# Performance work log

Hardware: AMD Instinct MI355X
Metric: run time of the kernel (lower is better)

## Reference

```python
import jax, jax.numpy as jnp
import numpy as np
import math

B, T, D = 2, 4096, 1024
H = 16
HEAD_DIM = D // H
CHUNK = 64

def setup_inputs() -> dict:
    key = jax.random.key(0)
    ks = jax.random.split(key, 9)
    s = 1.0 / math.sqrt(D)
    return {
        'x':  jax.random.normal(ks[0], (B, T, D), dtype=jnp.float32),
        'Wq': jax.random.normal(ks[1], (D, D), dtype=jnp.float32) * s,
        'bq': jax.random.normal(ks[2], (D,), dtype=jnp.float32) * 0.01,
        'Wk': jax.random.normal(ks[3], (D, D), dtype=jnp.float32) * s,
        'bk': jax.random.normal(ks[4], (D,), dtype=jnp.float32) * 0.01,
        'Wv': jax.random.normal(ks[5], (D, D), dtype=jnp.float32) * s,
        'bv': jax.random.normal(ks[6], (D,), dtype=jnp.float32) * 0.01,
        'Wo': jax.random.normal(ks[7], (D, D), dtype=jnp.float32) * s,
        'bo': jax.random.normal(ks[8], (D,), dtype=jnp.float32) * 0.01,
    }

def chunked_attention(q, k, v, chunk_size, scale):
    # q,k,v: (B,H,T,hd); causal Q-chunked attention, chunk_size divides T
    Bq, Hq, Tq, hd = q.shape
    S = k.shape[2]
    nc = Tq // chunk_size
    # (nc, B, H, chunk, hd)
    q_chunks = q.reshape(Bq, Hq, nc, chunk_size, hd).transpose(2, 0, 1, 3, 4)
    starts = jnp.arange(nc, dtype=jnp.int32) * chunk_size
    k_pos = jnp.arange(S)

    def body(carry, xs):
        qc, start = xs  # qc: (B,H,chunk,hd)
        scores = jnp.einsum('bhqd,bhkd->bhqk', qc, k) * scale  # (B,H,chunk,S)
        q_pos = start + jnp.arange(chunk_size)
        causal_mask = k_pos[None, :] > q_pos[:, None]  # (chunk,S)
        scores = jnp.where(causal_mask[None, None], -jnp.inf, scores)
        m = jnp.max(scores, axis=-1, keepdims=True)
        m = jnp.where(jnp.isinf(m), jnp.zeros_like(m), m)
        p = jax.nn.softmax(scores - m, axis=-1)
        oc = jnp.einsum('bhqk,bhkd->bhqd', p, v)
        return carry, oc

    _, outs = jax.lax.scan(body, None, (q_chunks, starts))  # (nc,B,H,chunk,hd)
    return outs.transpose(1, 2, 0, 3, 4).reshape(Bq, Hq, Tq, hd)

def reference(x, Wq, bq, Wk, bk, Wv, bv, Wo, bo):
    Bx, Tx, Dx = x.shape
    scale = 1.0 / math.sqrt(HEAD_DIM)

    def proj(W, b):
        y = x @ W.T + b  # torch Linear convention
        return y.reshape(Bx, Tx, H, HEAD_DIM).transpose(0, 2, 1, 3)

    q = proj(Wq, bq)
    k = proj(Wk, bk)
    v = proj(Wv, bv)
    out = chunked_attention(q, k, v, CHUNK, scale)  # (B,H,T,hd)
    out = out.transpose(0, 2, 1, 3).reshape(Bx, Tx, Dx)
    return out @ Wo.T + bo
```

## Files before the change

### kernel.cpp

```cpp
#include <hip/hip_runtime.h>
#include <math.h>

#define B_  2
#define T_  4096
#define D_  1024
#define H_  16
#define HD_ 64
#define M_  8192

using f32x4  = __attribute__((ext_vector_type(4)))  float;
using f32x16 = __attribute__((ext_vector_type(16))) float;
using bfrag  = __attribute__((ext_vector_type(8)))  short;

__device__ __forceinline__ unsigned short f2bf(float f) {
  union { float f; unsigned u; } v; v.f = f;
  unsigned r = v.u + 0x7FFFu + ((v.u >> 16) & 1u);
  return (unsigned short)(r >> 16);
}

__device__ __forceinline__ unsigned cvt_pk(float lo, float hi) {
  unsigned r;
  asm("v_cvt_pk_bf16_f32 %0, %1, %2" : "=v"(r) : "v"(lo), "v"(hi));
  return r;
}

__device__ __forceinline__ void plswap(unsigned &a, unsigned &b) {
  asm("v_permlane32_swap_b32 %0, %1" : "+v"(a), "+v"(b));
}

__device__ __forceinline__ void async16(const void* g, void* l) {
  __builtin_amdgcn_global_load_lds(
      (const __attribute__((address_space(1))) unsigned int*)g,
      (__attribute__((address_space(3))) unsigned int*)l, 16, 0, 0);
}

__global__ __launch_bounds__(256) void convert_all(
    const float* __restrict__ x, const float* __restrict__ wq,
    const float* __restrict__ wk, const float* __restrict__ wv,
    const float* __restrict__ wo, unsigned short* __restrict__ dst)
{
  const size_t NX = (size_t)M_ * D_ / 4;
  const size_t NW = (size_t)D_ * D_ / 4;
  const size_t total = NX + 4 * NW;
  size_t i = (size_t)blockIdx.x * blockDim.x + threadIdx.x;
  size_t stride = (size_t)gridDim.x * blockDim.x;
  for (size_t v = i; v < total; v += stride) {
    const float4* src;
    if (v < NX) {
      src = (const float4*)x + v;
    } else {
      size_t j = v - NX;
      const float* wp = (j < NW) ? wq : (j < 2*NW) ? wk : (j < 3*NW) ? wv : wo;
      src = (const float4*)wp + (j & (NW - 1));
    }
    float4 f = *src;
    ushort4 u;
    u.x = f2bf(f.x); u.y = f2bf(f.y); u.z = f2bf(f.z); u.w = f2bf(f.w);
    *(ushort4*)(dst + v * 4) = u;
  }
}

__global__ __launch_bounds__(256) void gemm_qkv(
    const unsigned short* __restrict__ A,
    const unsigned short* __restrict__ Ww,
    const float* __restrict__ bq, const float* __restrict__ bk,
    const float* __restrict__ bv,
    unsigned short* __restrict__ Qb, unsigned short* __restrict__ Kb,
    unsigned short* __restrict__ Vtb, float qscale)
{
  __shared__ unsigned short a_t[128 * 64];
  __shared__ unsigned short b_t[128 * 64];
  const int tid = threadIdx.x;
  const int lane = tid & 63;
  const int w = tid >> 6;
  const int lo = lane & 15, hi = lane >> 4;
  const int mbase = blockIdx.x * 128;
  const int nbase = blockIdx.y * 128;
  const int wm = w >> 1, wn = w & 1;
  const int K = D_;

  f32x4 acc[4][4];
  #pragma unroll
  for (int m = 0; m < 4; m++)
    #pragma unroll
    for (int n = 0; n < 4; n++) acc[m][n] = f32x4{0.f, 0.f, 0.f, 0.f};

  for (int k0 = 0; k0 < K; k0 += 64) {
    #pragma unroll
    for (int i = 0; i < 4; i++) {
      const int cb = i * 256 + w * 64;
      const int chunk = cb + lane;
      const int row = chunk >> 3, c8 = chunk & 7;
      async16(A  + (size_t)(mbase + row) * K + k0 + c8 * 8, &a_t[cb * 8]);
      async16(Ww + (size_t)(nbase + row) * K + k0 + c8 * 8, &b_t[cb * 8]);
    }
    __syncthreads();
    #pragma unroll
    for (int kk = 0; kk < 2; kk++) {
      bfrag af[4], bf[4];
      #pragma unroll
      for (int m = 0; m < 4; m++)
        af[m] = *(const bfrag*)&a_t[(wm * 64 + m * 16 + lo) * 64 + kk * 32 + hi * 8];
      #pragma unroll
      for (int n = 0; n < 4; n++)
        bf[n] = *(const bfrag*)&b_t[(wn * 64 + n * 16 + lo) * 64 + kk * 32 + hi * 8];
      #pragma unroll
      for (int m = 0; m < 4; m++)
        #pragma unroll
        for (int n = 0; n < 4; n++)
          acc[m][n] = __builtin_amdgcn_mfma_f32_16x16x32_bf16(af[m], bf[n], acc[m][n], 0, 0, 0);
    }
    __syncthreads();
  }

  const int which = nbase >> 10;
  const float* bias = (which == 0) ? bq : (which == 1) ? bk : bv;
  const float osc = (which == 0) ? qscale : 1.0f;
  const int nloc = nbase & 1023;

  float bvv[4];
  #pragma unroll
  for (int n = 0; n < 4; n++) bvv[n] = bias[nloc + wn * 64 + n * 16 + lo];

  #pragma unroll
  for (int m = 0; m < 4; m++) {
    const int rowl = wm * 64 + m * 16 + hi * 4;
    #pragma unroll
    for (int n = 0; n < 4; n++) {
      const int gn = nloc + wn * 64 + n * 16 + lo;
      const int h = gn >> 6, d = gn & 63;
      #pragma unroll
      for (int i = 0; i < 4; i++) {
        const float v = (acc[m][n][i] + bvv[n]) * osc;
        const int gm = mbase + rowl + i;
        const int b = gm >> 12, t = gm & 4095;
        const int bh = b * H_ + h;
        if (which == 0) {
          Qb[(((size_t)bh * T_) + t) * HD_ + d] = f2bf(v);
        } else if (which == 1) {
          const int j = t >> 6, kh = (t >> 5) & 1, l31r = t & 31;
          const int s = d >> 4, h5 = (d >> 3) & 1, e = d & 7;
          Kb[(((size_t)(bh * 64 + j) * 8 + kh * 4 + s) * 512)
             + l31r * 16 + h5 * 8 + e] = f2bf(v);
        } else {
          const int j = t >> 6, kh = (t >> 5) & 1, S = (t >> 4) & 1;
          const int h5 = (t >> 3) & 1, e = t & 7;
          const int dset = d >> 5, l31r = d & 31;
          Vtb[(((size_t)(bh * 64 + j) * 8 + kh * 4 + S * 2 + dset) * 512)
              + l31r * 16 + h5 * 8 + e] = f2bf(v);
        }
      }
    }
  }
}

__global__ __launch_bounds__(256) void gemm_out(
    const unsigned short* __restrict__ A,
    const unsigned short* __restrict__ Bw,
    const float* __restrict__ bias,
    float* __restrict__ out,
    int M, int N, int K)
{
  __shared__ unsigned short a_t[128 * 64];
  __shared__ unsigned short b_t[128 * 64];
  const int tid = threadIdx.x;
  const int lane = tid & 63;
  const int w = tid >> 6;
  const int lo = lane & 15, hi = lane >> 4;
  const int mbase = blockIdx.x * 128;
  const int nbase = blockIdx.y * 128;
  const int wm = w >> 1, wn = w & 1;

  f32x4 acc[4][4];
  #pragma unroll
  for (int m = 0; m < 4; m++)
    #pragma unroll
    for (int n = 0; n < 4; n++) acc[m][n] = f32x4{0.f, 0.f, 0.f, 0.f};

  for (int k0 = 0; k0 < K; k0 += 64) {
    #pragma unroll
    for (int i = 0; i < 4; i++) {
      const int cb = i * 256 + w * 64;
      const int chunk = cb + lane;
      const int row = chunk >> 3, c8 = chunk & 7;
      async16(A  + (size_t)(mbase + row) * K + k0 + c8 * 8, &a_t[cb * 8]);
      async16(Bw + (size_t)(nbase + row) * K + k0 + c8 * 8, &b_t[cb * 8]);
    }
    __syncthreads();
    #pragma unroll
    for (int kk = 0; kk < 2; kk++) {
      bfrag af[4], bf[4];
      #pragma unroll
      for (int m = 0; m < 4; m++)
        af[m] = *(const bfrag*)&a_t[(wm * 64 + m * 16 + lo) * 64 + kk * 32 + hi * 8];
      #pragma unroll
      for (int n = 0; n < 4; n++)
        bf[n] = *(const bfrag*)&b_t[(wn * 64 + n * 16 + lo) * 64 + kk * 32 + hi * 8];
      #pragma unroll
      for (int m = 0; m < 4; m++)
        #pragma unroll
        for (int n = 0; n < 4; n++)
          acc[m][n] = __builtin_amdgcn_mfma_f32_16x16x32_bf16(af[m], bf[n], acc[m][n], 0, 0, 0);
    }
    __syncthreads();
  }

  float bvv[4];
  #pragma unroll
  for (int n = 0; n < 4; n++) bvv[n] = bias[nbase + wn * 64 + n * 16 + lo];

  #pragma unroll
  for (int m = 0; m < 4; m++) {
    const int rowl = wm * 64 + m * 16 + hi * 4;
    #pragma unroll
    for (int n = 0; n < 4; n++) {
      const int gn = nbase + wn * 64 + n * 16 + lo;
      #pragma unroll
      for (int i = 0; i < 4; i++)
        out[(size_t)(mbase + rowl + i) * N + gn] = acc[m][n][i] + bvv[n];
    }
  }
}

__global__ __launch_bounds__(256, 3) void attn_kernel(
    const unsigned short* __restrict__ Qg,
    const unsigned short* __restrict__ Kf,
    const unsigned short* __restrict__ Vf,
    unsigned short* __restrict__ Og)
{
  __shared__ float smrg[2176];
  const int tid = threadIdx.x, lane = tid & 63, w = tid >> 6;
  const int l31 = lane & 31, hi5 = lane >> 5;
  const int bh = blockIdx.x & 31;
  const int qgroup = 63 - (blockIdx.x >> 5);
  const int qhalf = w >> 1, khalf = w & 1;
  const int a = qgroup * 2 + qhalf;
  const int qg_lane = qgroup * 64 + qhalf * 32 + l31;
  const int jw = (a >= khalf) ? ((a - khalf) >> 1) : -1;
  const int b = bh >> 4, h = bh & 15;

  bfrag qf0, qf1, qf2, qf3;
  {
    const unsigned short* qp = Qg + ((size_t)bh * T_ + qg_lane) * HD_ + hi5 * 8;
    qf0 = *(const bfrag*)(qp);
    qf1 = *(const bfrag*)(qp + 16);
    qf2 = *(const bfrag*)(qp + 32);
    qf3 = *(const bfrag*)(qp + 48);
  }

  const int loff = l31 * 16 + hi5 * 8;
  const unsigned short* kp =
      Kf + ((size_t)(bh * 64) * 8 + khalf * 4) * 512 + loff;
  const unsigned short* vp =
      Vf + ((size_t)(bh * 64) * 8 + khalf * 4) * 512 + loff;

  f32x16 o0, o1;
  #pragma unroll
  for (int r = 0; r < 16; r++) { o0[r] = 0.f; o1[r] = 0.f; }
  float l = 0.f;

  bfrag kA0, kA1, kA2, kA3, kB0, kB1, kB2, kB3;
  bfrag vf00, vf01, vf10, vf11;

  #define LOADK(P) do {                                                      \
    P##0 = *(const bfrag*)(kp);                                              \
    P##1 = *(const bfrag*)(kp + 512);                                        \
    P##2 = *(const bfrag*)(kp + 1024);                                       \
    P##3 = *(const bfrag*)(kp + 1536);                                       \
    kp += 4096;                                                              \
  } while (0)

  #define LOADV() do {                                                       \
    vf00 = *(const bfrag*)(vp);                                              \
    vf01 = *(const bfrag*)(vp + 512);                                        \
    vf10 = *(const bfrag*)(vp + 1024);                                       \
    vf11 = *(const bfrag*)(vp + 1536);                                       \
    vp += 4096;                                                              \
  } while (0)

  #define COMPUTE(P, J) do {                                                 \
    f32x16 st;                                                               \
    _Pragma("unroll")                                                        \
    for (int r = 0; r < 16; r++) st[r] = 0.f;                                \
    __builtin_amdgcn_s_setprio(1);                                           \
    st = __builtin_amdgcn_mfma_f32_32x32x16_bf16(P##0, qf0, st, 0, 0, 0);    \
    st = __builtin_amdgcn_mfma_f32_32x32x16_bf16(P##1, qf1, st, 0, 0, 0);    \
    st = __builtin_amdgcn_mfma_f32_32x32x16_bf16(P##2, qf2, st, 0, 0, 0);    \
    st = __builtin_amdgcn_mfma_f32_32x32x16_bf16(P##3, qf3, st, 0, 0, 0);    \
    __builtin_amdgcn_s_setprio(0);                                           \
    if ((J) == jw) {                                                         \
      const int thr = qg_lane - 64 * (J) - 32 * khalf - 4 * hi5;             \
      _Pragma("unroll")                                                      \
      for (int r = 0; r < 16; r++) {                                         \
        const int kl = (r & 3) + 8 * (r >> 2);                               \
        st[r] = (kl > thr) ? -INFINITY : st[r];                              \
      }                                                                      \
    }                                                                        \
    _Pragma("unroll")                                                        \
    for (int r = 0; r < 16; r++) st[r] = exp2f(st[r]);                       \
    {                                                                        \
      float s8[8];                                                           \
      _Pragma("unroll")                                                      \
      for (int r = 0; r < 8; r++) s8[r] = st[r] + st[r + 8];                 \
      float rs = ((s8[0] + s8[4]) + (s8[1] + s8[5])) +                       \
                 ((s8[2] + s8[6]) + (s8[3] + s8[7]));                        \
      rs += __shfl_xor(rs, 32);                                              \
      l += rs;                                                               \
    }                                                                        \
    {                                                                        \
      unsigned pk0 = cvt_pk(st[0], st[1]);                                   \
      unsigned pk1 = cvt_pk(st[2], st[3]);                                   \
      unsigned pk2 = cvt_pk(st[4], st[5]);                                   \
      unsigned pk3 = cvt_pk(st[6], st[7]);                                   \
      plswap(pk0, pk2);                                                      \
      plswap(pk1, pk3);                                                      \
      union { unsigned u[4]; bfrag f; } pb;                                  \
      pb.u[0] = pk0; pb.u[1] = pk1; pb.u[2] = pk2; pb.u[3] = pk3;            \
      __builtin_amdgcn_s_setprio(1);                                         \
      o0 = __builtin_amdgcn_mfma_f32_32x32x16_bf16(vf00, pb.f, o0, 0, 0, 0); \
      o1 = __builtin_amdgcn_mfma_f32_32x32x16_bf16(vf01, pb.f, o1, 0, 0, 0); \
      __builtin_amdgcn_s_setprio(0);                                         \
      pk0 = cvt_pk(st[8], st[9]);                                            \
      pk1 = cvt_pk(st[10], st[11]);                                          \
      pk2 = cvt_pk(st[12], st[13]);                                          \
      pk3 = cvt_pk(st[14], st[15]);                                          \
      plswap(pk0, pk2);                                                      \
      plswap(pk1, pk3);                                                      \
      pb.u[0] = pk0; pb.u[1] = pk1; pb.u[2] = pk2; pb.u[3] = pk3;            \
      __builtin_amdgcn_s_setprio(1);                                         \
      o0 = __builtin_amdgcn_mfma_f32_32x32x16_bf16(vf10, pb.f, o0, 0, 0, 0); \
      o1 = __builtin_amdgcn_mfma_f32_32x32x16_bf16(vf11, pb.f, o1, 0, 0, 0); \
      __builtin_amdgcn_s_setprio(0);                                         \
    }                                                                        \
  } while (0)

  if (jw >= 0) {
    LOADK(kA);
    int j = 0;
    while (true) {
      LOADV();
      if (j < jw) LOADK(kB);
      COMPUTE(kA, j);
      ++j; if (j > jw) break;
      LOADV();
      if (j < jw) LOADK(kA);
      COMPUTE(kB, j);
      ++j; if (j > jw) break;
    }
  }
  #undef LOADK
  #undef LOADV
  #undef COMPUTE

  const int moff = (qhalf * 64 + lane) * 17;
  if (khalf) {
    #pragma unroll
    for (int r = 0; r < 16; r++) smrg[moff + r] = o0[r];
    smrg[moff + 16] = l;
  }
  __syncthreads();
  if (!khalf) {
    #pragma unroll
    for (int r = 0; r < 16; r++) o0[r] += smrg[moff + r];
    l += smrg[moff + 16];
  }
  __syncthreads();
  if (khalf) {
    #pragma unroll
    for (int r = 0; r < 16; r++) smrg[moff + r] = o1[r];
  }
  __syncthreads();
  if (!khalf) {
    #pragma unroll
    for (int r = 0; r < 16; r++) o1[r] += smrg[moff + r];
    const float inv = 1.0f / l;
    unsigned short* orow = Og + ((size_t)(b * T_ + qg_lane)) * D_ + h * HD_;
    #pragma unroll
    for (int r = 0; r < 16; r += 2) {
      const int d0 = (r & 3) + 8 * (r >> 2) + 4 * hi5;
      unsigned u0 = cvt_pk(o0[r] * inv, o0[r + 1] * inv);
      unsigned u1 = cvt_pk(o1[r] * inv, o1[r + 1] * inv);
      *(unsigned*)(orow + d0)      = u0;
      *(unsigned*)(orow + 32 + d0) = u1;
    }
  }
}

extern "C" void kernel_launch(void* const* d_in, const int* in_sizes, int n_in,
                              void* d_out, int out_size, void* d_ws, size_t ws_size,
                              hipStream_t stream)
{
  const float* x  = (const float*)d_in[0];
  const float* Wq = (const float*)d_in[1];
  const float* bq = (const float*)d_in[2];
  const float* Wk = (const float*)d_in[3];
  const float* bk = (const float*)d_in[4];
  const float* Wv = (const float*)d_in[5];
  const float* bv = (const float*)d_in[6];
  const float* Wo = (const float*)d_in[7];
  const float* bo = (const float*)d_in[8];

  unsigned short* ws  = (unsigned short*)d_ws;
  unsigned short* xb  = ws;
  unsigned short* wqb = xb  + (size_t)M_ * D_;
  unsigned short* wkb = wqb + (size_t)D_ * D_;
  unsigned short* wvb = wkb + (size_t)D_ * D_;
  unsigned short* wob = wvb + (size_t)D_ * D_;
  unsigned short* Qb  = wob + (size_t)D_ * D_;
  unsigned short* Kb  = Qb  + (size_t)M_ * D_;
  unsigned short* Vtb = Kb  + (size_t)M_ * D_;
  unsigned short* AOb = Vtb + (size_t)M_ * D_;

  convert_all<<<2048, 256, 0, stream>>>(x, Wq, Wk, Wv, Wo, xb);

  const float qscale = 0.125f * 1.44269504f;
  dim3 gq(M_ / 128, 3072 / 128);
  gemm_qkv<<<gq, 256, 0, stream>>>(xb, wqb, bq, bk, bv, Qb, Kb, Vtb, qscale);

  attn_kernel<<<2048, 256, 0, stream>>>(Qb, Kb, Vtb, AOb);

  dim3 go(M_ / 128, D_ / 128);
  gemm_out<<<go, 256, 0, stream>>>(AOb, wob, bo, (float*)d_out, M_, D_, D_);
}
```

Before: 242.1 us.

## Software-pipeline QK MFMA ahead of softmax/PV in attention loop

Restructures the attention inner loop so the QK^T MFMAs for the next key block are issued before the softmax and PV MFMAs of the current block. This lets matrix work overlap with the exp/convert VALU work. The causal mask is applied only to the final block, outside the steady-state loop, and the row-sum cross-half shuffle is deferred to one shuffle after the loop. Launch bounds are raised to 4 blocks per CU and the double-buffered K registers are dropped to save VGPRs. The risk is register spilling or extra loads of K past the last needed block.

```diff
diff --git a/kernel.cpp b/kernel.cpp
--- a/kernel.cpp
+++ b/kernel.cpp
@@ -28,11 +28,13 @@
   asm("v_permlane32_swap_b32 %0, %1" : "+v"(a), "+v"(b));
 }
 
+
 __device__ __forceinline__ void async16(const void* g, void* l) {
   __builtin_amdgcn_global_load_lds(
       (const __attribute__((address_space(1))) unsigned int*)g,
       (__attribute__((address_space(3))) unsigned int*)l, 16, 0, 0);
 }
+
 
 __global__ __launch_bounds__(256) void convert_all(
     const float* __restrict__ x, const float* __restrict__ wq,
@@ -222,7 +224,7 @@
   }
 }
 
-__global__ __launch_bounds__(256, 3) void attn_kernel(
+__global__ __launch_bounds__(256, 4) void attn_kernel(
     const unsigned short* __restrict__ Qg,
     const unsigned short* __restrict__ Kf,
     const unsigned short* __restrict__ Vf,
@@ -259,14 +261,14 @@
   for (int r = 0; r < 16; r++) { o0[r] = 0.f; o1[r] = 0.f; }
   float l = 0.f;
 
-  bfrag kA0, kA1, kA2, kA3, kB0, kB1, kB2, kB3;
+  bfrag kA0, kA1, kA2, kA3;
   bfrag vf00, vf01, vf10, vf11;
 
-  #define LOADK(P) do {                                                      \
-    P##0 = *(const bfrag*)(kp);                                              \
-    P##1 = *(const bfrag*)(kp + 512);                                        \
-    P##2 = *(const bfrag*)(kp + 1024);                                       \
-    P##3 = *(const bfrag*)(kp + 1536);                                       \
+  #define LOADK() do {                                                       \
+    kA0 = *(const bfrag*)(kp);                                               \
+    kA1 = *(const bfrag*)(kp + 512);                                         \
+    kA2 = *(const bfrag*)(kp + 1024);                                        \
+    kA3 = *(const bfrag*)(kp + 1536);                                        \
     kp += 4096;                                                              \
   } while (0)
 
@@ -278,40 +280,40 @@
     vp += 4096;                                                              \
   } while (0)
 
-  #define COMPUTE(P, J) do {                                                 \
-    f32x16 st;                                                               \
+  #define QKSTEP(ST) do {                                                    \
+    __builtin_amdgcn_s_setprio(1);                                           \
+    ST = __builtin_amdgcn_mfma_f32_32x32x16_bf16(kA0, qf0,                   \
+                                                 (f32x16)(0.0f), 0, 0, 0);   \
+    ST = __builtin_amdgcn_mfma_f32_32x32x16_bf16(kA1, qf1, ST, 0, 0, 0);     \
+    ST = __builtin_amdgcn_mfma_f32_32x32x16_bf16(kA2, qf2, ST, 0, 0, 0);     \
+    ST = __builtin_amdgcn_mfma_f32_32x32x16_bf16(kA3, qf3, ST, 0, 0, 0);     \
+    __builtin_amdgcn_s_setprio(0);                                           \
+  } while (0)
+
+  #define MASK(ST) do {                                                     \
+    const int thr = qg_lane - 64 * jw - 32 * khalf - 4 * hi5;                \
     _Pragma("unroll")                                                        \
-    for (int r = 0; r < 16; r++) st[r] = 0.f;                                \
-    __builtin_amdgcn_s_setprio(1);                                           \
-    st = __builtin_amdgcn_mfma_f32_32x32x16_bf16(P##0, qf0, st, 0, 0, 0);    \
-    st = __builtin_amdgcn_mfma_f32_32x32x16_bf16(P##1, qf1, st, 0, 0, 0);    \
-    st = __builtin_amdgcn_mfma_f32_32x32x16_bf16(P##2, qf2, st, 0, 0, 0);    \
-    st = __builtin_amdgcn_mfma_f32_32x32x16_bf16(P##3, qf3, st, 0, 0, 0);    \
-    __builtin_amdgcn_s_setprio(0);                                           \
-    if ((J) == jw) {                                                         \
-      const int thr = qg_lane - 64 * (J) - 32 * khalf - 4 * hi5;             \
-      _Pragma("unroll")                                                      \
-      for (int r = 0; r < 16; r++) {                                         \
-        const int kl = (r & 3) + 8 * (r >> 2);                               \
-        st[r] = (kl > thr) ? -INFINITY : st[r];                              \
-      }                                                                      \
+    for (int r = 0; r < 16; r++) {                                           \
+      const int kl = (r & 3) + 8 * (r >> 2);                                 \
+      ST[r] = (kl > thr) ? -INFINITY : ST[r];                                \
     }                                                                        \
+  } while (0)
+
+  #define SOFTPV(ST) do {                                                    \
     _Pragma("unroll")                                                        \
-    for (int r = 0; r < 16; r++) st[r] = exp2f(st[r]);                       \
+    for (int r = 0; r < 16; r++) ST[r] = exp2f(ST[r]);                       \
     {                                                                        \
       float s8[8];                                                           \
       _Pragma("unroll")                                                      \
-      for (int r = 0; r < 8; r++) s8[r] = st[r] + st[r + 8];                 \
-      float rs = ((s8[0] + s8[4]) + (s8[1] + s8[5])) +                       \
-                 ((s8[2] + s8[6]) + (s8[3] + s8[7]));                        \
-      rs += __shfl_xor(rs, 32);                                              \
-      l += rs;                                                               \
+      for (int r = 0; r < 8; r++) s8[r] = ST[r] + ST[r + 8];                 \
+      l += ((s8[0] + s8[4]) + (s8[1] + s8[5])) +                             \
+           ((s8[2] + s8[6]) + (s8[3] + s8[7]));                              \
     }                                                                        \
     {                                                                        \
-      unsigned pk0 = cvt_pk(st[0], st[1]);                                   \
-      unsigned pk1 = cvt_pk(st[2], st[3]);                                   \
-      unsigned pk2 = cvt_pk(st[4], st[5]);                                   \
-      unsigned pk3 = cvt_pk(st[6], st[7]);                                   \
+      unsigned pk0 = cvt_pk(ST[0], ST[1]);                                   \
+      unsigned pk1 = cvt_pk(ST[2], ST[3]);                                   \
+      unsigned pk2 = cvt_pk(ST[4], ST[5]);                                   \
+      unsigned pk3 = cvt_pk(ST[6], ST[7]);                                   \
       plswap(pk0, pk2);                                                      \
       plswap(pk1, pk3);                                                      \
       union { unsigned u[4]; bfrag f; } pb;                                  \
@@ -320,10 +322,10 @@
       o0 = __builtin_amdgcn_mfma_f32_32x32x16_bf16(vf00, pb.f, o0, 0, 0, 0); \
       o1 = __builtin_amdgcn_mfma_f32_32x32x16_bf16(vf01, pb.f, o1, 0, 0, 0); \
       __builtin_amdgcn_s_setprio(0);                                         \
-      pk0 = cvt_pk(st[8], st[9]);                                            \
-      pk1 = cvt_pk(st[10], st[11]);                                          \
-      pk2 = cvt_pk(st[12], st[13]);                                          \
-      pk3 = cvt_pk(st[14], st[15]);                                          \
+      pk0 = cvt_pk(ST[8], ST[9]);                                            \
+      pk1 = cvt_pk(ST[10], ST[11]);                                          \
+      pk2 = cvt_pk(ST[12], ST[13]);                                          \
+      pk3 = cvt_pk(ST[14], ST[15]);                                          \
       plswap(pk0, pk2);                                                      \
       plswap(pk1, pk3);                                                      \
       pb.u[0] = pk0; pb.u[1] = pk1; pb.u[2] = pk2; pb.u[3] = pk3;            \
@@ -335,22 +337,32 @@
   } while (0)
 
   if (jw >= 0) {
-    LOADK(kA);
+    f32x16 stA, stB;
+    LOADK();
+    LOADV();
+    QKSTEP(stA);
+    LOADK();
     int j = 0;
-    while (true) {
-      LOADV();
-      if (j < jw) LOADK(kB);
-      COMPUTE(kA, j);
-      ++j; if (j > jw) break;
-      LOADV();
-      if (j < jw) LOADK(kA);
-      COMPUTE(kB, j);
-      ++j; if (j > jw) break;
+    while (j + 2 <= jw) {
+      QKSTEP(stB); LOADK(); SOFTPV(stA); LOADV(); ++j;
+      QKSTEP(stA); LOADK(); SOFTPV(stB); LOADV(); ++j;
+    }
+    if (j < jw) {
+      QKSTEP(stB); LOADK(); SOFTPV(stA); LOADV(); ++j;
+      MASK(stB);
+      SOFTPV(stB);
+    } else {
+      MASK(stA);
+      SOFTPV(stA);
     }
   }
   #undef LOADK
   #undef LOADV
-  #undef COMPUTE
+  #undef QKSTEP
+  #undef MASK
+  #undef SOFTPV
+
+  l += __shfl_xor(l, 32);
 
   const int moff = (qhalf * 64 + lane) * 17;
   if (khalf) {
```

Result: slower. 892.9 us (+268.8%).
